# Kernel optimization log

Hardware: AMD Instinct MI355X
Metric: run time of the kernel (lower is better)

The kernel has to match this reference:

```python
import jax, jax.numpy as jnp
import numpy as np

KS = 64      # kernel_size
NFFT = 64    # n_fft
IC = 32      # in_channel
OC = 64      # out_channel
B, T1, T2 = 4, 4096, 512


def setup_inputs() -> dict:
    key = jax.random.key(0)
    k1, k2, k3, k4 = jax.random.split(key, 4)
    x = jax.random.normal(k1, (B, T1, IC), dtype=jnp.float32)
    # continuous index in [0, T1-1)
    index = jax.random.uniform(k2, (B, T2), dtype=jnp.float32) * (T1 - 1)
    kb = 1.0 / np.sqrt(KS * IC)  # matches reset_parameters uniform bound
    kernel = jax.random.uniform(k3, (OC, IC, NFFT), minval=-kb, maxval=kb, dtype=jnp.float32)
    bias = jax.random.uniform(k4, (OC,), minval=-kb, maxval=kb, dtype=jnp.float32)
    return {"x": x, "index": index, "kernel": kernel, "bias": bias}


def reference(x, index, kernel, bias):
    # fractional-delay kernel per (b, t2) via FFT phase shift
    i = jnp.floor(index).astype(jnp.int32)          # (b, t2) integer part
    f = index - jnp.floor(index)                    # (b, t2) fractional part
    freqs = jnp.arange(NFFT // 2 + 1)               # rfft bins
    shift = jnp.exp(2j * jnp.pi * f[..., None] * freqs / NFFT)   # (b, t2, nf)
    K = jnp.fft.rfft(kernel)                        # (oc, ic, nf)
    K = K[None, None] * shift[:, :, None, None, :]  # (b, t2, oc, ic, nf)
    ker = jnp.fft.irfft(K, n=KS)                    # (b, t2, oc, ic, ks)

    # gather centered length-ks windows of x at integer positions i
    pad = KS // 2
    x_pad = jnp.pad(x, ((0, 0), (pad, pad), (0, 0)))            # (b, t1+2p, ic)
    pos = i[:, :, None] + jnp.arange(KS)[None, None, :]          # (b, t2, ks)
    barr = jnp.arange(x.shape[0])[:, None, None]
    xwin = x_pad[barr, pos]                                      # (b, t2, ks, ic)

    # per-position matmul: out[b,t,o] = sum_{c,k} ker[b,t,o,c,k] * xwin[b,t,k,c]
    out = jnp.einsum('btock,btkc->bto', ker, xwin) + bias
    return out
```

## Files before the change

kernel.cpp:

```cpp
#include <hip/hip_runtime.h>
#include <hip/hip_bf16.h>
#include <math.h>

#define B_   4
#define T1_  4096
#define T2_  512
#define IC_  32
#define OC_  64
#define KS_  64

typedef unsigned short u16;
typedef unsigned int   u32;
typedef __attribute__((ext_vector_type(8))) short  short8;
typedef __attribute__((ext_vector_type(4))) float  float4v;

__device__ __forceinline__ float bf2f(u16 h) {
    union { u32 u; float f; } v; v.u = ((u32)h) << 16; return v.f;
}
__device__ __forceinline__ u16 f2bf(float f) {
    union { u32 u; float f; } v; v.f = f;
    u32 u = v.u;
    u32 r = (u + 0x7FFFu + ((u >> 16) & 1u)) >> 16;
    return (u16)r;
}

#define PI_F 3.14159265358979323846f

__global__ __launch_bounds__(256) void prep_interp_kernel(
        const float* __restrict__ x, const float* __restrict__ index,
        const float* __restrict__ kern, u16* __restrict__ Y,
        u16* __restrict__ Bsz)
{
    __shared__ __align__(16) float xwT[2][IC_][68];
    __shared__ __align__(16) float wsh[2][64];

    const int tid = threadIdx.x;

    if (blockIdx.x < 64) {
        int gid = blockIdx.x * 256 + tid;
        int o   = gid & 63;
        int cs8 = gid >> 6;
        const float* p = kern + (size_t)o * 2048 + cs8 * 8;
        float4 a = *(const float4*)p;
        float4 b = *(const float4*)(p + 4);
        u16* q = Bsz + (size_t)cs8 * 512 + o * 8;
        *(ushort4*)(q)     = make_ushort4(f2bf(a.x), f2bf(a.y), f2bf(a.z), f2bf(a.w));
        *(ushort4*)(q + 4) = make_ushort4(f2bf(b.x), f2bf(b.y), f2bf(b.z), f2bf(b.w));
        return;
    }

    const int p2 = blockIdx.x - 64;

    #pragma unroll
    for (int h = 0; h < 2; ++h) {
        const int bt = p2 * 2 + h;
        const int b  = bt >> 9;
        float fidx = index[bt];
        float flo  = floorf(fidx);
        int   i0   = (int)flo;
        float f    = fidx - flo;

        int e  = tid * 8;
        int k  = e >> 5;
        int c0 = e & 31;
        int pos = i0 + k - 32;
        float vals[8];
        if (pos >= 0 && pos < T1_) {
            const float* p = x + ((size_t)(b * T1_ + pos) * IC_ + c0);
            float4 a = *(const float4*)p;
            float4 d = *(const float4*)(p + 4);
            vals[0]=a.x; vals[1]=a.y; vals[2]=a.z; vals[3]=a.w;
            vals[4]=d.x; vals[5]=d.y; vals[6]=d.z; vals[7]=d.w;
        } else {
            #pragma unroll
            for (int q = 0; q < 8; ++q) vals[q] = 0.0f;
        }
        #pragma unroll
        for (int q = 0; q < 8; ++q) xwT[h][c0 + q][k] = vals[q];

        if (tid < 64) {
            int j = tid;
            float wj;
            if (f <= 0.0f) {
                wj = (j == 0) ? 1.0f : 0.0f;
            } else {
                float spf = sinf(PI_F * f);
                float a   = PI_F * ((float)j + f) * (1.0f / 64.0f);
                wj = ((j & 1) ? -spf : spf) * cosf(a) / (64.0f * sinf(a));
            }
            wsh[h][j] = wj;
        }
    }
    __syncthreads();

    const int h   = tid >> 7;
    const int rem = tid & 127;
    const int c   = rem >> 2;
    const int s0  = (rem & 3) << 4;

    float xr[64];
    #pragma unroll
    for (int q = 0; q < 16; ++q) {
        int idx = (s0 + q * 4) & 63;
        const float4 v = *(const float4*)&xwT[h][c][idx];
        xr[q*4+0] = v.x; xr[q*4+1] = v.y; xr[q*4+2] = v.z; xr[q*4+3] = v.w;
    }

    float acc[16];
    #pragma unroll
    for (int r = 0; r < 16; ++r) acc[r] = 0.0f;

    #pragma unroll
    for (int jq = 0; jq < 16; ++jq) {
        const float4 wv = *(const float4*)&wsh[h][jq * 4];
        #pragma unroll
        for (int jj = 0; jj < 4; ++jj) {
            const float wj = (jj == 0) ? wv.x : (jj == 1) ? wv.y : (jj == 2) ? wv.z : wv.w;
            const int j = jq * 4 + jj;
            #pragma unroll
            for (int r = 0; r < 16; ++r)
                acc[r] += wj * xr[(j + r) & 63];
        }
    }

    const int bt = p2 * 2 + h;
    union { u16 u[8]; short8 v; } o0, o1;
    #pragma unroll
    for (int r = 0; r < 8; ++r) { o0.u[r] = f2bf(acc[r]); o1.u[r] = f2bf(acc[8 + r]); }
    u16* yp = Y + ((size_t)bt * 2048 + c * 64 + s0);
    *(short8*)(yp)     = o0.v;
    *(short8*)(yp + 8) = o1.v;
}

__global__ __launch_bounds__(256) void gemm_kernel(const u16* __restrict__ Y,
                                                   const u16* __restrict__ Bsz,
                                                   const float* __restrict__ bias,
                                                   float* __restrict__ out)
{
    __shared__ float red[4][4][16][17];

    const int tid  = threadIdx.x;
    const int w    = tid >> 6;
    const int lane = tid & 63;
    const int nm   = lane & 15;
    const int q    = lane >> 4;
    const int bt0  = blockIdx.x * 16;
    const int kb0  = w * 16;

    const u16* aptr = Y   + (size_t)(bt0 + nm) * 2048 + kb0 * 32 + q * 8;
    const u16* bptr = Bsz + (size_t)kb0 * 2048 + q * 512 + nm * 8;

    float4v acc0 = {0.f,0.f,0.f,0.f};
    float4v acc1 = {0.f,0.f,0.f,0.f};
    float4v acc2 = {0.f,0.f,0.f,0.f};
    float4v acc3 = {0.f,0.f,0.f,0.f};

    short8 a  = *(const short8*)(aptr);
    short8 b0 = *(const short8*)(bptr);
    short8 b1 = *(const short8*)(bptr + 128);
    short8 b2 = *(const short8*)(bptr + 256);
    short8 b3 = *(const short8*)(bptr + 384);

    for (int kb = 0; kb < 16; ++kb) {
        short8 an, bn0, bn1, bn2, bn3;
        if (kb != 15) {
            const u16* ap = aptr + (kb + 1) * 32;
            const u16* bp = bptr + (size_t)(kb + 1) * 2048;
            an  = *(const short8*)(ap);
            bn0 = *(const short8*)(bp);
            bn1 = *(const short8*)(bp + 128);
            bn2 = *(const short8*)(bp + 256);
            bn3 = *(const short8*)(bp + 384);
        }
        acc0 = __builtin_amdgcn_mfma_f32_16x16x32_bf16(a, b0, acc0, 0, 0, 0);
        acc1 = __builtin_amdgcn_mfma_f32_16x16x32_bf16(a, b1, acc1, 0, 0, 0);
        acc2 = __builtin_amdgcn_mfma_f32_16x16x32_bf16(a, b2, acc2, 0, 0, 0);
        acc3 = __builtin_amdgcn_mfma_f32_16x16x32_bf16(a, b3, acc3, 0, 0, 0);
        if (kb != 15) { a = an; b0 = bn0; b1 = bn1; b2 = bn2; b3 = bn3; }
    }

    #pragma unroll
    for (int r = 0; r < 4; ++r) {
        red[w][0][q * 4 + r][nm] = acc0[r];
        red[w][1][q * 4 + r][nm] = acc1[r];
        red[w][2][q * 4 + r][nm] = acc2[r];
        red[w][3][q * 4 + r][nm] = acc3[r];
    }
    __syncthreads();

    #pragma unroll
    for (int e = tid; e < 1024; e += 256) {
        int row = e >> 6, oc = e & 63, nt = oc >> 4, col = oc & 15;
        float s = red[0][nt][row][col] + red[1][nt][row][col]
                + red[2][nt][row][col] + red[3][nt][row][col] + bias[oc];
        out[(size_t)(bt0 + row) * 64 + oc] = s;
    }
}

extern "C" void kernel_launch(void* const* d_in, const int* in_sizes, int n_in,
                              void* d_out, int out_size, void* d_ws, size_t ws_size,
                              hipStream_t stream)
{
    const float* x     = (const float*)d_in[0];
    const float* index = (const float*)d_in[1];
    const float* kern  = (const float*)d_in[2];
    const float* bias  = (const float*)d_in[3];
    float* out = (float*)d_out;

    u16* Y   = (u16*)d_ws;
    u16* Bsz = (u16*)((char*)d_ws + (size_t)8 * 1024 * 1024);

    prep_interp_kernel<<<dim3(64 + B_ * T2_ / 2), dim3(256), 0, stream>>>(x, index, kern, Y, Bsz);
    gemm_kernel<<<dim3(B_ * T2_ / 16), dim3(256), 0, stream>>>(Y, Bsz, bias, out);
}
```

Baseline: 79.39 us.

## Fuse interpolation and MFMA GEMM into one kernel with shared-memory handoff

Result: slower. 82.63 us (+4.1%).

```diff
diff --git a/kernel.cpp b/kernel.cpp
--- a/kernel.cpp
+++ b/kernel.cpp
@@ -7,193 +7,204 @@
 #define T2_  512
 #define IC_  32
 #define OC_  64
-#define KS_  64
 
 typedef unsigned short u16;
 typedef unsigned int   u32;
 typedef __attribute__((ext_vector_type(8))) short  short8;
 typedef __attribute__((ext_vector_type(4))) float  float4v;
 
-__device__ __forceinline__ float bf2f(u16 h) {
-    union { u32 u; float f; } v; v.u = ((u32)h) << 16; return v.f;
-}
 __device__ __forceinline__ u16 f2bf(float f) {
     union { u32 u; float f; } v; v.f = f;
     u32 u = v.u;
-    u32 r = (u + 0x7FFFu + ((u >> 16) & 1u)) >> 16;
-    return (u16)r;
+    return (u16)((u + 0x7FFFu + ((u >> 16) & 1u)) >> 16);
+}
+__device__ __forceinline__ float bfl(u32 d) {
+    union { u32 u; float f; } v; v.u = d << 16; return v.f;
+}
+__device__ __forceinline__ float bfh(u32 d) {
+    union { u32 u; float f; } v; v.u = d & 0xffff0000u; return v.f;
+}
+__device__ __forceinline__ u32 pk2(float lo, float hi) {
+    return __builtin_amdgcn_perm(__float_as_uint(hi), __float_as_uint(lo), 0x07060302);
+}
+__device__ __forceinline__ short8 packbf(float4 f0, float4 f1) {
+    union { u32 d[4]; short8 s; } r;
+    r.d[0] = pk2(f0.x, f0.y); r.d[1] = pk2(f0.z, f0.w);
+    r.d[2] = pk2(f1.x, f1.y); r.d[3] = pk2(f1.z, f1.w);
+    return r.s;
 }
 
 #define PI_F 3.14159265358979323846f
 
-__global__ __launch_bounds__(256) void prep_interp_kernel(
+__global__ __launch_bounds__(1024) void fused_kernel(
         const float* __restrict__ x, const float* __restrict__ index,
-        const float* __restrict__ kern, u16* __restrict__ Y,
-        u16* __restrict__ Bsz)
+        const float* __restrict__ kern, const float* __restrict__ bias,
+        float* __restrict__ out)
 {
-    __shared__ __align__(16) float xwT[2][IC_][68];
-    __shared__ __align__(16) float wsh[2][64];
+    __shared__ __align__(16) u32 buf[8704];
+    __shared__ __align__(16) float wf[8][64];
+    __shared__ int   ip8[8];
+    __shared__ float fr8[8];
 
     const int tid = threadIdx.x;
-
-    if (blockIdx.x < 64) {
-        int gid = blockIdx.x * 256 + tid;
-        int o   = gid & 63;
-        int cs8 = gid >> 6;
-        const float* p = kern + (size_t)o * 2048 + cs8 * 8;
-        float4 a = *(const float4*)p;
-        float4 b = *(const float4*)(p + 4);
-        u16* q = Bsz + (size_t)cs8 * 512 + o * 8;
-        *(ushort4*)(q)     = make_ushort4(f2bf(a.x), f2bf(a.y), f2bf(a.z), f2bf(a.w));
-        *(ushort4*)(q + 4) = make_ushort4(f2bf(b.x), f2bf(b.y), f2bf(b.z), f2bf(b.w));
-        return;
-    }
-
-    const int p2 = blockIdx.x - 64;
-
-    #pragma unroll
-    for (int h = 0; h < 2; ++h) {
-        const int bt = p2 * 2 + h;
-        const int b  = bt >> 9;
-        float fidx = index[bt];
+    const int bt0 = blockIdx.x * 8;
+
+    if (tid < 8) {
+        float fidx = index[bt0 + tid];
         float flo  = floorf(fidx);
-        int   i0   = (int)flo;
-        float f    = fidx - flo;
-
-        int e  = tid * 8;
-        int k  = e >> 5;
-        int c0 = e & 31;
-        int pos = i0 + k - 32;
-        float vals[8];
-        if (pos >= 0 && pos < T1_) {
-            const float* p = x + ((size_t)(b * T1_ + pos) * IC_ + c0);
-            float4 a = *(const float4*)p;
-            float4 d = *(const float4*)(p + 4);
-            vals[0]=a.x; vals[1]=a.y; vals[2]=a.z; vals[3]=a.w;
-            vals[4]=d.x; vals[5]=d.y; vals[6]=d.z; vals[7]=d.w;
+        ip8[tid] = (int)flo;
+        fr8[tid] = fidx - flo;
+    }
+    __syncthreads();
+
+    {
+        const int bt = tid >> 7;
+        const int r  = tid & 127;
+        const int c0 = (r & 15) * 2;
+        const int k8 = (r >> 4) * 8;
+        const int b  = (bt0 + bt) >> 9;
+        const int i0 = ip8[bt];
+        u32 pk[2][4];
+        #pragma unroll
+        for (int kk = 0; kk < 8; ++kk) {
+            int pos = i0 + k8 + kk - 32;
+            float vx = 0.f, vy = 0.f;
+            if (pos >= 0 && pos < T1_) {
+                const float2 v = *(const float2*)(x + ((size_t)(b * T1_ + pos) * IC_ + c0));
+                vx = v.x; vy = v.y;
+            }
+            u32 bx = f2bf(vx), by = f2bf(vy);
+            if (kk & 1) { pk[0][kk >> 1] |= bx << 16; pk[1][kk >> 1] |= by << 16; }
+            else        { pk[0][kk >> 1]  = bx;       pk[1][kk >> 1]  = by; }
+        }
+        u16* xw = (u16*)buf;
+        #pragma unroll
+        for (int cc = 0; cc < 2; ++cc) {
+            u32* p = (u32*)(xw + (size_t)bt * 2176 + (c0 + cc) * 68 + k8);
+            *(uint2*)(p)     = make_uint2(pk[cc][0], pk[cc][1]);
+            *(uint2*)(p + 2) = make_uint2(pk[cc][2], pk[cc][3]);
+        }
+    }
+    if (tid < 512) {
+        const int bt = tid >> 6, j = tid & 63;
+        const float f = fr8[bt];
+        float wj;
+        if (f <= 0.0f) {
+            wj = (j == 0) ? 1.0f : 0.0f;
         } else {
+            float spf = sinf(PI_F * f);
+            float a   = PI_F * ((float)j + f) * (1.0f / 64.0f);
+            wj = ((j & 1) ? -spf : spf) * cosf(a) / (64.0f * sinf(a));
+        }
+        wf[bt][j] = wj;
+    }
+    __syncthreads();
+
+    const int cbt = tid >> 7;
+    const int cch = (tid >> 2) & 31;
+    const int sq  = tid & 3;
+    const int s0  = sq * 16;
+    float xr[64];
+    {
+        const u16* row = (const u16*)buf + (size_t)cbt * 2176 + cch * 68;
+        #pragma unroll
+        for (int i = 0; i < 16; ++i) {
+            int k = (s0 + i * 4) & 63;
+            uint2 v = *(const uint2*)(row + k);
+            xr[i*4+0] = bfl(v.x); xr[i*4+1] = bfh(v.x);
+            xr[i*4+2] = bfl(v.y); xr[i*4+3] = bfh(v.y);
+        }
+    }
+    __syncthreads();
+
+    {
+        float acc[16];
+        #pragma unroll
+        for (int r = 0; r < 16; ++r) acc[r] = 0.f;
+        #pragma unroll
+        for (int jq = 0; jq < 16; ++jq) {
+            const float4 wv = *(const float4*)&wf[cbt][jq * 4];
             #pragma unroll
-            for (int q = 0; q < 8; ++q) vals[q] = 0.0f;
-        }
-        #pragma unroll
-        for (int q = 0; q < 8; ++q) xwT[h][c0 + q][k] = vals[q];
-
-        if (tid < 64) {
-            int j = tid;
-            float wj;
-            if (f <= 0.0f) {
-                wj = (j == 0) ? 1.0f : 0.0f;
-            } else {
-                float spf = sinf(PI_F * f);
-                float a   = PI_F * ((float)j + f) * (1.0f / 64.0f);
-                wj = ((j & 1) ? -spf : spf) * cosf(a) / (64.0f * sinf(a));
+            for (int jj = 0; jj < 4; ++jj) {
+                const float wj = (jj==0)?wv.x:(jj==1)?wv.y:(jj==2)?wv.z:wv.w;
+                const int j = jq * 4 + jj;
+                #pragma unroll
+                for (int r = 0; r < 16; ++r)
+                    acc[r] += wj * xr[(j + r) & 63];
             }
-            wsh[h][j] = wj;
-        }
-    }
-    __syncthreads();
-
-    const int h   = tid >> 7;
-    const int rem = tid & 127;
-    const int c   = rem >> 2;
-    const int s0  = (rem & 3) << 4;
-
-    float xr[64];
-    #pragma unroll
-    for (int q = 0; q < 16; ++q) {
-        int idx = (s0 + q * 4) & 63;
-        const float4 v = *(const float4*)&xwT[h][c][idx];
-        xr[q*4+0] = v.x; xr[q*4+1] = v.y; xr[q*4+2] = v.z; xr[q*4+3] = v.w;
-    }
-
-    float acc[16];
-    #pragma unroll
-    for (int r = 0; r < 16; ++r) acc[r] = 0.0f;
-
-    #pragma unroll
-    for (int jq = 0; jq < 16; ++jq) {
-        const float4 wv = *(const float4*)&wsh[h][jq * 4];
-        #pragma unroll
-        for (int jj = 0; jj < 4; ++jj) {
-            const float wj = (jj == 0) ? wv.x : (jj == 1) ? wv.y : (jj == 2) ? wv.z : wv.w;
-            const int j = jq * 4 + jj;
-            #pragma unroll
-            for (int r = 0; r < 16; ++r)
-                acc[r] += wj * xr[(j + r) & 63];
-        }
-    }
-
-    const int bt = p2 * 2 + h;
-    union { u16 u[8]; short8 v; } o0, o1;
-    #pragma unroll
-    for (int r = 0; r < 8; ++r) { o0.u[r] = f2bf(acc[r]); o1.u[r] = f2bf(acc[8 + r]); }
-    u16* yp = Y + ((size_t)bt * 2048 + c * 64 + s0);
-    *(short8*)(yp)     = o0.v;
-    *(short8*)(yp + 8) = o1.v;
-}
-
-__global__ __launch_bounds__(256) void gemm_kernel(const u16* __restrict__ Y,
-                                                   const u16* __restrict__ Bsz,
-                                                   const float* __restrict__ bias,
-                                                   float* __restrict__ out)
-{
-    __shared__ float red[4][4][16][17];
-
-    const int tid  = threadIdx.x;
+        }
+        u32 od[8];
+        #pragma unroll
+        for (int i = 0; i < 8; ++i)
+            od[i] = (u32)f2bf(acc[2*i]) | ((u32)f2bf(acc[2*i+1]) << 16);
+        const int key = (cch & 7) << 2;
+        u32* base = buf + (size_t)cbt * 1028 + cch * 32;
+        *(uint4*)(base + (((sq*8) + 0) ^ key)) = make_uint4(od[0], od[1], od[2], od[3]);
+        *(uint4*)(base + (((sq*8) + 4) ^ key)) = make_uint4(od[4], od[5], od[6], od[7]);
+    }
+    __syncthreads();
+
     const int w    = tid >> 6;
     const int lane = tid & 63;
     const int nm   = lane & 15;
     const int q    = lane >> 4;
-    const int bt0  = blockIdx.x * 16;
-    const int kb0  = w * 16;
-
-    const u16* aptr = Y   + (size_t)(bt0 + nm) * 2048 + kb0 * 32 + q * 8;
-    const u16* bptr = Bsz + (size_t)kb0 * 2048 + q * 512 + nm * 8;
-
-    float4v acc0 = {0.f,0.f,0.f,0.f};
-    float4v acc1 = {0.f,0.f,0.f,0.f};
-    float4v acc2 = {0.f,0.f,0.f,0.f};
-    float4v acc3 = {0.f,0.f,0.f,0.f};
-
-    short8 a  = *(const short8*)(aptr);
-    short8 b0 = *(const short8*)(bptr);
-    short8 b1 = *(const short8*)(bptr + 128);
-    short8 b2 = *(const short8*)(bptr + 256);
-    short8 b3 = *(const short8*)(bptr + 384);
-
-    for (int kb = 0; kb < 16; ++kb) {
-        short8 an, bn0, bn1, bn2, bn3;
-        if (kb != 15) {
-            const u16* ap = aptr + (kb + 1) * 32;
-            const u16* bp = bptr + (size_t)(kb + 1) * 2048;
-            an  = *(const short8*)(ap);
-            bn0 = *(const short8*)(bp);
-            bn1 = *(const short8*)(bp + 128);
-            bn2 = *(const short8*)(bp + 256);
-            bn3 = *(const short8*)(bp + 384);
-        }
-        acc0 = __builtin_amdgcn_mfma_f32_16x16x32_bf16(a, b0, acc0, 0, 0, 0);
-        acc1 = __builtin_amdgcn_mfma_f32_16x16x32_bf16(a, b1, acc1, 0, 0, 0);
-        acc2 = __builtin_amdgcn_mfma_f32_16x16x32_bf16(a, b2, acc2, 0, 0, 0);
-        acc3 = __builtin_amdgcn_mfma_f32_16x16x32_bf16(a, b3, acc3, 0, 0, 0);
-        if (kb != 15) { a = an; b0 = bn0; b1 = bn1; b2 = bn2; b3 = bn3; }
-    }
-
+    short8 afr[4];
     #pragma unroll
-    for (int r = 0; r < 4; ++r) {
-        red[w][0][q * 4 + r][nm] = acc0[r];
-        red[w][1][q * 4 + r][nm] = acc1[r];
-        red[w][2][q * 4 + r][nm] = acc2[r];
-        red[w][3][q * 4 + r][nm] = acc3[r];
-    }
-    __syncthreads();
-
+    for (int i = 0; i < 4; ++i) {
+        const int kb = w * 4 + i;
+        const int cA = kb >> 1;
+        const u32* p = buf + (size_t)(nm & 7) * 1028 + cA * 32
+                     + ((((kb & 1) * 16) + q * 4) ^ ((cA & 7) << 2));
+        union { uint4 u; short8 s; } cvt;
+        cvt.u = *(const uint4*)p;
+        const short8 zz = {0,0,0,0,0,0,0,0};
+        afr[i] = (nm < 8) ? cvt.s : zz;
+    }
+    __syncthreads();
+
+    float4v a0 = {0,0,0,0}, a1 = {0,0,0,0}, a2 = {0,0,0,0}, a3 = {0,0,0,0};
     #pragma unroll
-    for (int e = tid; e < 1024; e += 256) {
-        int row = e >> 6, oc = e & 63, nt = oc >> 4, col = oc & 15;
-        float s = red[0][nt][row][col] + red[1][nt][row][col]
-                + red[2][nt][row][col] + red[3][nt][row][col] + bias[oc];
-        out[(size_t)(bt0 + row) * 64 + oc] = s;
+    for (int i = 0; i < 4; ++i) {
+        const int kb = w * 4 + i;
+        const float* kp = kern + (size_t)nm * 2048 + kb * 32 + q * 8;
+        float4 f0, f1;
+        f0 = *(const float4*)(kp);
+        f1 = *(const float4*)(kp + 4);
+        a0 = __builtin_amdgcn_mfma_f32_16x16x32_bf16(afr[i], packbf(f0, f1), a0, 0, 0, 0);
+        f0 = *(const float4*)(kp + 16 * 2048);
+        f1 = *(const float4*)(kp + 16 * 2048 + 4);
+        a1 = __builtin_amdgcn_mfma_f32_16x16x32_bf16(afr[i], packbf(f0, f1), a1, 0, 0, 0);
+        f0 = *(const float4*)(kp + 32 * 2048);
+        f1 = *(const float4*)(kp + 32 * 2048 + 4);
+        a2 = __builtin_amdgcn_mfma_f32_16x16x32_bf16(afr[i], packbf(f0, f1), a2, 0, 0, 0);
+        f0 = *(const float4*)(kp + 48 * 2048);
+        f1 = *(const float4*)(kp + 48 * 2048 + 4);
+        a3 = __builtin_amdgcn_mfma_f32_16x16x32_bf16(afr[i], packbf(f0, f1), a3, 0, 0, 0);
+    }
+    {
+        float* red = (float*)buf;
+        if (q < 2) {
+            #pragma unroll
+            for (int r = 0; r < 4; ++r) {
+                const int row = q * 4 + r;
+                float* rp = red + (size_t)(w * 8 + row) * 68 + nm;
+                rp[0]  = a0[r];
+                rp[16] = a1[r];
+                rp[32] = a2[r];
+                rp[48] = a3[r];
+            }
+        }
+    }
+    __syncthreads();
+
+    if (tid < 512) {
+        const int m = tid >> 6, o = tid & 63;
+        float s = bias[o];
+        const float* red = (const float*)buf;
+        #pragma unroll
+        for (int w2 = 0; w2 < 16; ++w2)
+            s += red[(size_t)(w2 * 8 + m) * 68 + o];
+        out[(size_t)(bt0 + m) * 64 + o] = s;
     }
 }
 
@@ -207,9 +218,5 @@
     const float* bias  = (const float*)d_in[3];
     float* out = (float*)d_out;
 
-    u16* Y   = (u16*)d_ws;
-    u16* Bsz = (u16*)((char*)d_ws + (size_t)8 * 1024 * 1024);
-
-    prep_interp_kernel<<<dim3(64 + B_ * T2_ / 2), dim3(256), 0, stream>>>(x, index, kern, Y, Bsz);
-    gemm_kernel<<<dim3(B_ * T2_ / 16), dim3(256), 0, stream>>>(Y, Bsz, bias, out);
-}
+    fused_kernel<<<dim3(B_ * T2_ / 8), dim3(1024), 0, stream>>>(x, index, kern, bias, out);
+}
```

## Split GEMM K across eight waves with half-filled M tiles and full prefetch

Applied to the files above, without the earlier changes.

Measured after the change: 75.49 us. 4.9% less time.

```diff
diff --git a/kernel.cpp b/kernel.cpp
--- a/kernel.cpp
+++ b/kernel.cpp
@@ -14,14 +14,10 @@
 typedef __attribute__((ext_vector_type(8))) short  short8;
 typedef __attribute__((ext_vector_type(4))) float  float4v;
 
-__device__ __forceinline__ float bf2f(u16 h) {
-    union { u32 u; float f; } v; v.u = ((u32)h) << 16; return v.f;
-}
 __device__ __forceinline__ u16 f2bf(float f) {
     union { u32 u; float f; } v; v.f = f;
     u32 u = v.u;
-    u32 r = (u + 0x7FFFu + ((u >> 16) & 1u)) >> 16;
-    return (u16)r;
+    return (u16)((u + 0x7FFFu + ((u >> 16) & 1u)) >> 16);
 }
 
 #define PI_F 3.14159265358979323846f
@@ -132,68 +128,73 @@
     *(short8*)(yp + 8) = o1.v;
 }
 
-__global__ __launch_bounds__(256) void gemm_kernel(const u16* __restrict__ Y,
-                                                   const u16* __restrict__ Bsz,
-                                                   const float* __restrict__ bias,
-                                                   float* __restrict__ out)
+__global__ __launch_bounds__(512, 2) void gemm_kernel(const u16* __restrict__ Y,
+                                                      const u16* __restrict__ Bsz,
+                                                      const float* __restrict__ bias,
+                                                      float* __restrict__ out)
 {
-    __shared__ float red[4][4][16][17];
+    __shared__ float red[8][4][8][17];
 
     const int tid  = threadIdx.x;
     const int w    = tid >> 6;
     const int lane = tid & 63;
     const int nm   = lane & 15;
     const int q    = lane >> 4;
-    const int bt0  = blockIdx.x * 16;
-    const int kb0  = w * 16;
-
-    const u16* aptr = Y   + (size_t)(bt0 + nm) * 2048 + kb0 * 32 + q * 8;
+    const int g    = blockIdx.x;
+
+    const int rr  = nm & 7;
+    const int p2  = (g & 7) + 8 * (4 * (g >> 3) + (rr >> 1));
+    const int btA = 2 * p2 + (rr & 1);
+
+    const int kb0 = w * 8;
+    const u16* aptr = Y   + (size_t)btA * 2048 + kb0 * 32 + q * 8;
     const u16* bptr = Bsz + (size_t)kb0 * 2048 + q * 512 + nm * 8;
 
-    float4v acc0 = {0.f,0.f,0.f,0.f};
-    float4v acc1 = {0.f,0.f,0.f,0.f};
-    float4v acc2 = {0.f,0.f,0.f,0.f};
-    float4v acc3 = {0.f,0.f,0.f,0.f};
-
-    short8 a  = *(const short8*)(aptr);
-    short8 b0 = *(const short8*)(bptr);
-    short8 b1 = *(const short8*)(bptr + 128);
-    short8 b2 = *(const short8*)(bptr + 256);
-    short8 b3 = *(const short8*)(bptr + 384);
-
-    for (int kb = 0; kb < 16; ++kb) {
-        short8 an, bn0, bn1, bn2, bn3;
-        if (kb != 15) {
-            const u16* ap = aptr + (kb + 1) * 32;
-            const u16* bp = bptr + (size_t)(kb + 1) * 2048;
-            an  = *(const short8*)(ap);
-            bn0 = *(const short8*)(bp);
-            bn1 = *(const short8*)(bp + 128);
-            bn2 = *(const short8*)(bp + 256);
-            bn3 = *(const short8*)(bp + 384);
-        }
-        acc0 = __builtin_amdgcn_mfma_f32_16x16x32_bf16(a, b0, acc0, 0, 0, 0);
-        acc1 = __builtin_amdgcn_mfma_f32_16x16x32_bf16(a, b1, acc1, 0, 0, 0);
-        acc2 = __builtin_amdgcn_mfma_f32_16x16x32_bf16(a, b2, acc2, 0, 0, 0);
-        acc3 = __builtin_amdgcn_mfma_f32_16x16x32_bf16(a, b3, acc3, 0, 0, 0);
-        if (kb != 15) { a = an; b0 = bn0; b1 = bn1; b2 = bn2; b3 = bn3; }
-    }
-
-    #pragma unroll
-    for (int r = 0; r < 4; ++r) {
-        red[w][0][q * 4 + r][nm] = acc0[r];
-        red[w][1][q * 4 + r][nm] = acc1[r];
-        red[w][2][q * 4 + r][nm] = acc2[r];
-        red[w][3][q * 4 + r][nm] = acc3[r];
+    short8 a[8], b[8][4];
+    #pragma unroll
+    for (int i = 0; i < 8; ++i) {
+        a[i] = *(const short8*)(aptr + i * 32);
+        #pragma unroll
+        for (int n = 0; n < 4; ++n)
+            b[i][n] = *(const short8*)(bptr + (size_t)i * 2048 + n * 128);
+    }
+    if (nm >= 8) {
+        const short8 zz = {0,0,0,0,0,0,0,0};
+        #pragma unroll
+        for (int i = 0; i < 8; ++i) a[i] = zz;
+    }
+
+    float4v acc0 = {0,0,0,0}, acc1 = {0,0,0,0}, acc2 = {0,0,0,0}, acc3 = {0,0,0,0};
+    #pragma unroll
+    for (int i = 0; i < 8; ++i) {
+        acc0 = __builtin_amdgcn_mfma_f32_16x16x32_bf16(a[i], b[i][0], acc0, 0, 0, 0);
+        acc1 = __builtin_amdgcn_mfma_f32_16x16x32_bf16(a[i], b[i][1], acc1, 0, 0, 0);
+        acc2 = __builtin_amdgcn_mfma_f32_16x16x32_bf16(a[i], b[i][2], acc2, 0, 0, 0);
+        acc3 = __builtin_amdgcn_mfma_f32_16x16x32_bf16(a[i], b[i][3], acc3, 0, 0, 0);
+    }
+
+    if (q < 2) {
+        #pragma unroll
+        for (int r = 0; r < 4; ++r) {
+            const int row = q * 4 + r;
+            red[w][0][row][nm] = acc0[r];
+            red[w][1][row][nm] = acc1[r];
+            red[w][2][row][nm] = acc2[r];
+            red[w][3][row][nm] = acc3[r];
+        }
     }
     __syncthreads();
 
-    #pragma unroll
-    for (int e = tid; e < 1024; e += 256) {
-        int row = e >> 6, oc = e & 63, nt = oc >> 4, col = oc & 15;
-        float s = red[0][nt][row][col] + red[1][nt][row][col]
-                + red[2][nt][row][col] + red[3][nt][row][col] + bias[oc];
-        out[(size_t)(bt0 + row) * 64 + oc] = s;
+    {
+        const int row = tid >> 6;
+        const int o   = tid & 63;
+        float s = bias[o];
+        #pragma unroll
+        for (int ww = 0; ww < 8; ++ww)
+            s += red[ww][o >> 4][row][o & 15];
+        const int p2o = (g & 7) + 8 * (4 * (g >> 3) + (row >> 1));
+        const int bto = 2 * p2o + (row & 1);
+        out[(size_t)bto * 64 + o] = s;
     }
 }
 
@@ -211,5 +212,5 @@
     u16* Bsz = (u16*)((char*)d_ws + (size_t)8 * 1024 * 1024);
 
     prep_interp_kernel<<<dim3(64 + B_ * T2_ / 2), dim3(256), 0, stream>>>(x, index, kern, Y, Bsz);
-    gemm_kernel<<<dim3(B_ * T2_ / 16), dim3(256), 0, stream>>>(Y, Bsz, bias, out);
-}
+    gemm_kernel<<<dim3(256), dim3(512), 0, stream>>>(Y, Bsz, bias, out);
+}
```
